# Performance work log

Hardware: AMD Instinct MI355X
Metric: run time of the kernel (lower is better)

## Reference

```python
import jax, jax.numpy as jnp
import numpy as np

B, S, H = 4, 8256, 768
NH, HD = 12, 64
W = 128
SHIFT = W // 2  # 64; first SHIFT tokens form their own block after the shift
NW = (S - SHIFT) // W  # 64 full windows
ROPE_BASE = 10000.0


def _rope_cos_sin(length, hd):
    inv_freq = 1.0 / (ROPE_BASE ** (jnp.arange(0, hd, 2, dtype=jnp.float32) / hd))
    ang = jnp.arange(length, dtype=jnp.float32)[:, None] * inv_freq[None, :]  # [L, hd/2]
    return jnp.cos(ang), jnp.sin(ang)


def _apply_rope(x, cos, sin):
    # x: [..., L, hd]; cos/sin: [L, hd/2] (broadcast over leading dims)
    x1, x2 = x[..., : HD // 2], x[..., HD // 2 :]
    return jnp.concatenate([x1 * cos - x2 * sin, x2 * cos + x1 * sin], axis=-1)


def _sdpa(q, k, v):
    # q,k,v: [..., L, hd]; full softmax attention within the block
    scores = jnp.einsum('...qd,...kd->...qk', q, k) / jnp.sqrt(jnp.asarray(HD, q.dtype))
    probs = jax.nn.softmax(scores, axis=-1)
    return jnp.einsum('...qk,...kd->...qd', probs, v)


def setup_inputs() -> dict:
    key = jax.random.key(0)
    ks = jax.random.split(key, 8)
    std = 0.02
    return {
        'hidden_states': jax.random.normal(ks[0], (B, S, H), dtype=jnp.float32),
        'attention_mask': jnp.zeros((B, 1, 1, S), dtype=jnp.float32),
        'Wq': jax.random.normal(ks[1], (H, H), dtype=jnp.float32) * std,
        'bq': jnp.zeros((H,), dtype=jnp.float32),
        'Wk': jax.random.normal(ks[2], (H, H), dtype=jnp.float32) * std,
        'bk': jnp.zeros((H,), dtype=jnp.float32),
        'Wv': jax.random.normal(ks[3], (H, H), dtype=jnp.float32) * std,
        'bv': jnp.zeros((H,), dtype=jnp.float32),
    }


def _global_block(h, Wq, bq, Wk, bk, Wv, bv):
    # h: [B, L, H]; full attention with global-position RoPE (BertSelfAttention.forward)
    L = h.shape[1]
    cos, sin = _rope_cos_sin(L, HD)

    def heads(x):  # [B, L, H] -> [B, NH, L, HD]
        return x.reshape(B, L, NH, HD).transpose(0, 2, 1, 3)

    q = _apply_rope(heads(h @ Wq.T + bq), cos, sin)
    k = _apply_rope(heads(h @ Wk.T + bk), cos, sin)
    v = heads(h @ Wv.T + bv)
    ctx = _sdpa(q, k, v)  # [B, NH, L, HD]
    return ctx.transpose(0, 2, 1, 3).reshape(B, L, H)


def _local_blocks(h, Wq, bq, Wk, bk, Wv, bv):
    # h: [B, NW*W, H]; per-window attention with window-local RoPE (_mh_local)
    cos, sin = _rope_cos_sin(W, HD)

    def win_heads(x):  # [B, NW*W, H] -> [B, NW, NH, W, HD]
        return x.reshape(B, NW, W, NH, HD).transpose(0, 1, 3, 2, 4)

    q = _apply_rope(win_heads(h @ Wq.T + bq), cos, sin)
    k = _apply_rope(win_heads(h @ Wk.T + bk), cos, sin)
    v = win_heads(h @ Wv.T + bv)
    ctx = _sdpa(q, k, v)  # [B, NW, NH, W, HD]
    return ctx.transpose(0, 1, 3, 2, 4).reshape(B, NW * W, H)


def reference(hidden_states, attention_mask, Wq, bq, Wk, bk, Wv, bv):
    # Shifted local attention: first SHIFT tokens attend among themselves
    # (small global block), the rest is split into NW full windows of size W.
    head = _global_block(hidden_states[:, :SHIFT, :], Wq, bq, Wk, bk, Wv, bv)
    body = _local_blocks(hidden_states[:, SHIFT:, :], Wq, bq, Wk, bk, Wv, bv)
    return jnp.concatenate([head, body], axis=1)  # [B, S, H]
```

## Files before the change

kernel.cpp:

```cpp
#include <hip/hip_runtime.h>
#include <stdint.h>

constexpr int B  = 4, S = 8256, H = 768, NH = 12, HD = 64;
constexpr int M  = B * S;
constexpr int N3 = 3 * H;
constexpr int NWG_GEMM = (M / 128) * (N3 / 128);
constexpr int XQ8 = NWG_GEMM / 8, XR8 = NWG_GEMM % 8;
constexpr long XB_OFF   = 0;
constexpr long XB_BYTES = (long)M * H * 2;
constexpr long W_OFF    = XB_OFF + XB_BYTES;
constexpr long W_BYTES  = (long)N3 * H * 2;
constexpr long ROPE_OFF = W_OFF + W_BYTES;
constexpr long ROPE_BYTES = 128 * 32 * 2 * 4;
constexpr long QKV_OFF  = ROPE_OFF + ROPE_BYTES;
constexpr long QKV_BYTES = (long)M * N3 * 2;
constexpr long WS_NEEDED = QKV_OFF + QKV_BYTES;

typedef __attribute__((ext_vector_type(8))) _Float16 h8;
typedef __attribute__((ext_vector_type(8))) unsigned short us8;
typedef __attribute__((ext_vector_type(4))) float f4;

#define MFMA16(a,b,c) __builtin_amdgcn_mfma_f32_16x16x32_f16((a),(b),(c),0,0,0)
#define GLL16(gp, lp) __builtin_amdgcn_global_load_lds( \
    (__attribute__((address_space(1))) void*)(gp),      \
    (__attribute__((address_space(3))) void*)(lp), 16, 0, 0)

static __device__ __forceinline__ unsigned short f2h(float x) {
  _Float16 h = (_Float16)x;
  return __builtin_bit_cast(unsigned short, h);
}
static __device__ __forceinline__ f4 f4z() { f4 z = {0.f,0.f,0.f,0.f}; return z; }

__global__ __launch_bounds__(256) void prep_kernel(
    const float* __restrict__ X,
    const float* __restrict__ Wq, const float* __restrict__ Wk, const float* __restrict__ Wv,
    unsigned short* __restrict__ Xb, unsigned short* __restrict__ Wcat, float* __restrict__ rope)
{
  int bid = blockIdx.x;
  if (bid < 12384) {
    long base = (long)bid * 2048 + threadIdx.x * 8;
    float4 v0 = *(const float4*)(X + base);
    float4 v1 = *(const float4*)(X + base + 4);
    us8 o;
    o[0]=f2h(v0.x); o[1]=f2h(v0.y); o[2]=f2h(v0.z); o[3]=f2h(v0.w);
    o[4]=f2h(v1.x); o[5]=f2h(v1.y); o[6]=f2h(v1.z); o[7]=f2h(v1.w);
    *(us8*)(Xb + base) = o;
  } else if (bid < 13248) {
    int wb  = bid - 12384;
    int mat = wb / 288;
    int base = (wb % 288) * 2048 + threadIdx.x * 8;
    const float* src = (mat == 0) ? Wq : (mat == 1) ? Wk : Wv;
    float4 v0 = *(const float4*)(src + base);
    float4 v1 = *(const float4*)(src + base + 4);
    us8 o;
    o[0]=f2h(v0.x); o[1]=f2h(v0.y); o[2]=f2h(v0.z); o[3]=f2h(v0.w);
    o[4]=f2h(v1.x); o[5]=f2h(v1.y); o[6]=f2h(v1.z); o[7]=f2h(v1.w);
    *(us8*)(Wcat + (long)mat * 589824 + base) = o;
  } else {
    int t = (bid - 13248) * 256 + threadIdx.x;
    int p = t >> 5, i = t & 31;
    double ang = (double)p * pow(10000.0, -(double)i / 32.0);
    rope[2*t]   = (float)cos(ang);
    rope[2*t+1] = (float)sin(ang);
  }
}

__global__ __launch_bounds__(256) void qkv_gemm(
    const unsigned short* __restrict__ Xb, const unsigned short* __restrict__ Wb,
    const float* __restrict__ bqp, const float* __restrict__ bkp, const float* __restrict__ bvp,
    const float* __restrict__ rope, unsigned short* __restrict__ QKV)
{
  __shared__ __align__(16) unsigned char ldsA[2][16384];
  __shared__ __align__(16) unsigned char ldsB[2][16384];
  const int tid = threadIdx.x, lane = tid & 63, wid = tid >> 6;

  const int bid0 = blockIdx.x;
  const int xcd = bid0 & 7, idx = bid0 >> 3;
  const int wgid = (xcd < XR8 ? xcd * (XQ8 + 1) : XR8 * (XQ8 + 1) + (xcd - XR8) * XQ8) + idx;
  const int mt = wgid / 18;
  const int nt = wgid % 18;
  const long m0 = (long)mt * 128;
  const int  n0 = nt * 128;
  const int wm = wid >> 1, wn = wid & 1;

  f4 acc[4][4];
  #pragma unroll
  for (int i = 0; i < 4; ++i)
    #pragma unroll
    for (int j = 0; j < 4; ++j) acc[i][j] = f4z();

  const char* Xc = (const char*)Xb;
  const char* Wc = (const char*)Wb;

#define STAGE(Abuf, Bbuf, kt) do {                                          \
    const int k0b_ = (kt) * 128;                                            \
    _Pragma("unroll")                                                       \
    for (int i_ = 0; i_ < 4; ++i_) {                                        \
      const int ob_ = ((i_ << 2) + wid) * 1024;      \
      const int o_  = ob_ + lane * 16;                \
      const int row_ = o_ >> 7, cb_ = o_ & 127;                             \
      const int csrc_ = cb_ ^ ((row_ & 7) << 4);      \
      GLL16(Xc + (m0 + row_) * 1536 + k0b_ + csrc_, (Abuf) + ob_);          \
      GLL16(Wc + (long)(n0 + row_) * 1536 + k0b_ + csrc_, (Bbuf) + ob_);    \
    }                                                                       \
  } while (0)

#define COMPUTE(Abuf, Bbuf) do {                                            \
    _Pragma("unroll")                                                       \
    for (int ks_ = 0; ks_ < 2; ++ks_) {                                     \
      h8 a_[4], b_[4];                                                      \
      const int kb_ = ks_ * 64 + ((lane >> 4) << 4);                        \
      _Pragma("unroll")                                                     \
      for (int f_ = 0; f_ < 4; ++f_) {                                      \
        const int ra_ = wm * 64 + f_ * 16 + (lane & 15);                    \
        a_[f_] = *(const h8*)((Abuf) + ra_ * 128 + (kb_ ^ ((ra_ & 7) << 4)));\
        const int rb_ = wn * 64 + f_ * 16 + (lane & 15);                    \
        b_[f_] = *(const h8*)((Bbuf) + rb_ * 128 + (kb_ ^ ((rb_ & 7) << 4)));\
      }                                                                     \
      _Pragma("unroll")                                                     \
      for (int fm_ = 0; fm_ < 4; ++fm_)                                     \
        _Pragma("unroll")                                                   \
        for (int fn_ = 0; fn_ < 4; ++fn_)                                   \
          acc[fm_][fn_] = MFMA16(a_[fm_], b_[fn_], acc[fm_][fn_]);          \
    }                                                                       \
  } while (0)

  unsigned char* A0 = ldsA[0];  unsigned char* A1 = ldsA[1];
  unsigned char* B0 = ldsB[0];  unsigned char* B1 = ldsB[1];

  STAGE(A0, B0, 0);
  #pragma unroll
  for (int kt = 0; kt < 12; kt += 2) {
    STAGE(A1, B1, kt + 1);
    asm volatile("s_waitcnt vmcnt(8)" ::: "memory");
    __builtin_amdgcn_s_barrier();
    asm volatile("" ::: "memory");
    COMPUTE(A0, B0);
    asm volatile("" ::: "memory");
    __builtin_amdgcn_s_barrier();
    if (kt + 2 < 12) {
      STAGE(A0, B0, kt + 2);
      asm volatile("s_waitcnt vmcnt(8)" ::: "memory");
    } else {
      asm volatile("s_waitcnt vmcnt(0)" ::: "memory");
    }
    __builtin_amdgcn_s_barrier();
    asm volatile("" ::: "memory");
    COMPUTE(A1, B1);
    asm volatile("" ::: "memory");
    __builtin_amdgcn_s_barrier();
  }
#undef STAGE
#undef COMPUTE

  const int colb = n0 + wn * 64;
  const int sel = (colb >= 1536) ? 2 : (colb >= 768) ? 1 : 0;
  const float* bias = (sel == 0) ? bqp : (sel == 1) ? bkp : bvp;
  const int hcol = colb % 768;
  float bia[4];
  #pragma unroll
  for (int f = 0; f < 4; ++f) bia[f] = bias[hcol + f * 16 + (lane & 15)];

  #pragma unroll
  for (int fm = 0; fm < 4; ++fm) {
    #pragma unroll
    for (int reg = 0; reg < 4; ++reg) {
      const long m = m0 + wm * 64 + fm * 16 + ((lane >> 4) << 2) + reg;
      const int s = (int)(m % (long)S);
      const int pos = (s < 64) ? s : ((s - 64) & 127);
      unsigned short* orow = QKV + m * N3 + colb;
      if (sel < 2) {
        #pragma unroll
        for (int f = 0; f < 2; ++f) {
          const int d1 = f * 16 + (lane & 15);
          const float c  = rope[(pos * 32 + d1) * 2];
          const float sn = rope[(pos * 32 + d1) * 2 + 1];
          const float x1 = acc[fm][f][reg]     + bia[f];
          const float x2 = acc[fm][f + 2][reg] + bia[f + 2];
          orow[f * 16 + (lane & 15)]       = f2h(x1 * c - x2 * sn);
          orow[(f + 2) * 16 + (lane & 15)] = f2h(x2 * c + x1 * sn);
        }
      } else {
        #pragma unroll
        for (int f = 0; f < 4; ++f)
          orow[f * 16 + (lane & 15)] = f2h(acc[fm][f][reg] + bia[f]);
      }
    }
  }
}

template <int T>
__global__ __launch_bounds__(256) void attn_kernel(
    const unsigned short* __restrict__ QKV, float* __restrict__ out)
{
  constexpr int NF  = T / 16;
  constexpr int NKS = T / 32;
  __shared__ __align__(16) unsigned char sKV[16384];
  __shared__ __align__(16) unsigned char sP[4][8192];

  const int tid = threadIdx.x, lane = tid & 63, w = tid >> 6;
  int bid = blockIdx.x;
  const int h = bid % NH; bid /= NH;
  long row0;
  if (T == 64) row0 = (long)bid * S;
  else { const int ww = bid % 64; const int b = bid / 64; row0 = (long)b * S + 64 + (long)ww * 128; }
  const unsigned short* Qb = QKV + row0 * N3 + h * HD;
  const unsigned short* Kb = Qb + H;
  const unsigned short* Vb = Qb + 2 * H;

  {
    const char* Kc = (const char*)Kb;
    #pragma unroll
    for (int i = 0; i < T / 32; ++i) {
      const int o = i * 4096 + tid * 16;
      const int row = o >> 7, cb = o & 127;
      const int csrc = cb ^ ((row & 7) << 4);
      GLL16(Kc + (long)row * (N3 * 2) + csrc, sKV + o);
    }
  }
  us8 va0, va1, vc0, vc1;
  const bool vload = (2 * lane + 1 < T);
  if (vload) {
    const unsigned short* v0 = Vb + (long)(2 * lane) * N3 + w * 16;
    const unsigned short* v1 = v0 + N3;
    va0 = *(const us8*)(v0);  va1 = *(const us8*)(v0 + 8);
    vc0 = *(const us8*)(v1);  vc1 = *(const us8*)(v1 + 8);
  }
  __syncthreads();

  const bool active = (w * 32 < T);
  f4 acc[2][NF];
  if (active) {
    h8 aq[2][2];
    #pragma unroll
    for (int fm = 0; fm < 2; ++fm)
      #pragma unroll
      for (int ks = 0; ks < 2; ++ks) {
        const long r = w * 32 + fm * 16 + (lane & 15);
        aq[fm][ks] = *(const h8*)(Qb + r * N3 + ks * 32 + ((lane >> 4) << 3));
      }
    #pragma unroll
    for (int i = 0; i < 2; ++i)
      #pragma unroll
      for (int f = 0; f < NF; ++f) acc[i][f] = f4z();

    const int kb0 = (lane >> 4) << 4;
    #pragma unroll
    for (int f = 0; f < NF; ++f) {
      const int rk = f * 16 + (lane & 15);
      const int base = rk * 128, sw = (rk & 7) << 4;
      h8 b0 = *(const h8*)(sKV + base + (kb0 ^ sw));
      h8 b1 = *(const h8*)(sKV + base + ((64 + kb0) ^ sw));
      acc[0][f] = MFMA16(aq[0][0], b0, acc[0][f]);
      acc[0][f] = MFMA16(aq[0][1], b1, acc[0][f]);
      acc[1][f] = MFMA16(aq[1][0], b0, acc[1][f]);
      acc[1][f] = MFMA16(aq[1][1], b1, acc[1][f]);
    }
  }
  __syncthreads();

  if (vload) {
    #pragma unroll
    for (int i = 0; i < 8; ++i) {
      const int d = w * 16 + i, d2 = d + 8;
      *(unsigned*)(sKV + d  * 256 + ((4 * lane) ^ ((d  & 15) << 4))) = (unsigned)va0[i] | ((unsigned)vc0[i] << 16);
      *(unsigned*)(sKV + d2 * 256 + ((4 * lane) ^ ((d2 & 15) << 4))) = (unsigned)va1[i] | ((unsigned)vc1[i] << 16);
    }
  }
  if (active) {
    unsigned char* Pw = sP[w];
    #pragma unroll
    for (int fm = 0; fm < 2; ++fm) {
      #pragma unroll
      for (int reg = 0; reg < 4; ++reg) {
        float mx = -3.0e38f;
        #pragma unroll
        for (int f = 0; f < NF; ++f) mx = fmaxf(mx, acc[fm][f][reg]);
        mx = fmaxf(mx, __shfl_xor(mx, 1));
        mx = fmaxf(mx, __shfl_xor(mx, 2));
        mx = fmaxf(mx, __shfl_xor(mx, 4));
        mx = fmaxf(mx, __shfl_xor(mx, 8));
        float pv[NF], sum = 0.f;
        #pragma unroll
        for (int f = 0; f < NF; ++f) {
          const float p = __expf((acc[fm][f][reg] - mx) * 0.125f);
          pv[f] = p; sum += p;
        }
        sum += __shfl_xor(sum, 1);
        sum += __shfl_xor(sum, 2);
        sum += __shfl_xor(sum, 4);
        sum += __shfl_xor(sum, 8);
        const float inv = 1.0f / sum;
        const int rloc = fm * 16 + ((lane >> 4) << 2) + reg;
        const int swz = (rloc & 7) << 4;
        #pragma unroll
        for (int f = 0; f < NF; ++f) {
          const int cb = (f * 16 + (lane & 15)) * 2;
          *(unsigned short*)(Pw + rloc * 256 + (cb ^ swz)) = f2h(pv[f] * inv);
        }
      }
    }
  }
  __syncthreads();

  if (active) {
    unsigned char* Pw = sP[w];
    f4 acc2[2][4];
    #pragma unroll
    for (int i = 0; i < 2; ++i)
      #pragma unroll
      for (int j = 0; j < 4; ++j) acc2[i][j] = f4z();

    #pragma unroll
    for (int ks = 0; ks < NKS; ++ks) {
      h8 pa[2], vb[4];
      const int kb = ks * 64 + ((lane >> 4) << 4);
      #pragma unroll
      for (int fm = 0; fm < 2; ++fm) {
        const int rp = fm * 16 + (lane & 15);
        pa[fm] = *(const h8*)(Pw + rp * 256 + (kb ^ ((rp & 7) << 4)));
      }
      #pragma unroll
      for (int df = 0; df < 4; ++df) {
        const int d = df * 16 + (lane & 15);
        vb[df] = *(const h8*)(sKV + d * 256 + (kb ^ ((d & 15) << 4)));
      }
      #pragma unroll
      for (int fm = 0; fm < 2; ++fm)
        #pragma unroll
        for (int df = 0; df < 4; ++df)
          acc2[fm][df] = MFMA16(pa[fm], vb[df], acc2[fm][df]);
    }

    float* ob = out + (row0 + w * 32) * H + h * HD;
    #pragma unroll
    for (int fm = 0; fm < 2; ++fm)
      #pragma unroll
      for (int df = 0; df < 4; ++df)
        #pragma unroll
        for (int reg = 0; reg < 4; ++reg) {
          const long r = fm * 16 + ((lane >> 4) << 2) + reg;
          const int c = df * 16 + (lane & 15);
          ob[r * H + c] = acc2[fm][df][reg];
        }
  }
}

extern "C" void kernel_launch(void* const* d_in, const int* in_sizes, int n_in,
                              void* d_out, int out_size, void* d_ws, size_t ws_size,
                              hipStream_t stream) {
  const float* X  = (const float*)d_in[0];
  const float* Wq = (const float*)d_in[2];
  const float* bq = (const float*)d_in[3];
  const float* Wk = (const float*)d_in[4];
  const float* bk = (const float*)d_in[5];
  const float* Wv = (const float*)d_in[6];
  const float* bv = (const float*)d_in[7];
  float* out = (float*)d_out;

  if ((long)ws_size < WS_NEEDED) return;

  char* ws = (char*)d_ws;
  unsigned short* Xb   = (unsigned short*)(ws + XB_OFF);
  unsigned short* Wcat = (unsigned short*)(ws + W_OFF);
  float*          rope = (float*)(ws + ROPE_OFF);
  unsigned short* QKV  = (unsigned short*)(ws + QKV_OFF);

  prep_kernel<<<13264, 256, 0, stream>>>(X, Wq, Wk, Wv, Xb, Wcat, rope);
  qkv_gemm<<<NWG_GEMM, 256, 0, stream>>>(Xb, Wcat, bq, bk, bv, rope, QKV);
  attn_kernel<64><<<B * NH, 256, 0, stream>>>(QKV, out);
  attn_kernel<128><<<B * 64 * NH, 256, 0, stream>>>(QKV, out);
}
```

Measured before the change: 399.9 us.

## Deepen QKV GEMM pipeline to five stages with 64-wide K tiles

The QKV projection GEMM moves from a double-buffered 128-wide K loop to a 5-buffer ring of 64-wide K tiles, keeping four tiles of loads in flight. The A and B tiles for each stage share one buffer, and a new row-pair swizzle keeps LDS reads conflict-free at the narrower width. The goal is to hide global-to-LDS load latency better. In exchange it uses more LDS (80KB vs 64KB), which may lower occupancy, and it does more barriers per unit of work.

```diff
diff --git a/kernel.cpp b/kernel.cpp
--- a/kernel.cpp
+++ b/kernel.cpp
@@ -24,6 +24,7 @@
 #define GLL16(gp, lp) __builtin_amdgcn_global_load_lds( \
     (__attribute__((address_space(1))) void*)(gp),      \
     (__attribute__((address_space(3))) void*)(lp), 16, 0, 0)
+#define WAITV(N) asm volatile("s_waitcnt vmcnt(" #N ")" ::: "memory")
 
 static __device__ __forceinline__ unsigned short f2h(float x) {
   _Float16 h = (_Float16)x;
@@ -70,8 +71,7 @@
     const float* __restrict__ bqp, const float* __restrict__ bkp, const float* __restrict__ bvp,
     const float* __restrict__ rope, unsigned short* __restrict__ QKV)
 {
-  __shared__ __align__(16) unsigned char ldsA[2][16384];
-  __shared__ __align__(16) unsigned char ldsB[2][16384];
+  __shared__ __align__(16) unsigned char lds[5][16384];
   const int tid = threadIdx.x, lane = tid & 63, wid = tid >> 6;
 
   const int bid0 = blockIdx.x;
@@ -92,61 +92,52 @@
   const char* Xc = (const char*)Xb;
   const char* Wc = (const char*)Wb;
 
-#define STAGE(Abuf, Bbuf, kt) do {                                          \
-    const int k0b_ = (kt) * 128;                                            \
+#define STAGE(bi, kt) do {                                                  \
+    const int k0b_ = (kt) * 64;                                             \
+    unsigned char* buf_ = lds[bi];                                          \
     _Pragma("unroll")                                                       \
-    for (int i_ = 0; i_ < 4; ++i_) {                                        \
-      const int ob_ = ((i_ << 2) + wid) * 1024;      \
-      const int o_  = ob_ + lane * 16;                \
-      const int row_ = o_ >> 7, cb_ = o_ & 127;                             \
-      const int csrc_ = cb_ ^ ((row_ & 7) << 4);      \
-      GLL16(Xc + (m0 + row_) * 1536 + k0b_ + csrc_, (Abuf) + ob_);          \
-      GLL16(Wc + (long)(n0 + row_) * 1536 + k0b_ + csrc_, (Bbuf) + ob_);    \
+    for (int i_ = 0; i_ < 2; ++i_) {                                        \
+      const int o_  = i_ * 4096 + tid * 16;           \
+      const int slot_ = o_ >> 7, d_ = o_ & 127;                             \
+      const int row_ = slot_ * 2 + (d_ >> 6), c_ = d_ & 63;                 \
+      const int cs_ = c_ ^ ((slot_ & 3) << 4);        \
+      GLL16(Xc + (m0 + row_) * 1536 + k0b_ + cs_, buf_ + o_);               \
+      GLL16(Wc + (long)(n0 + row_) * 1536 + k0b_ + cs_, buf_ + 8192 + o_);  \
     }                                                                       \
   } while (0)
 
-#define COMPUTE(Abuf, Bbuf) do {                                            \
+#define COMPUTE(bi) do {                                                    \
+    unsigned char* buf_ = lds[bi];                                          \
+    h8 a_[4], b_[4];                                                        \
+    const int kc_ = (lane >> 4) << 4;                                       \
     _Pragma("unroll")                                                       \
-    for (int ks_ = 0; ks_ < 2; ++ks_) {                                     \
-      h8 a_[4], b_[4];                                                      \
-      const int kb_ = ks_ * 64 + ((lane >> 4) << 4);                        \
+    for (int f_ = 0; f_ < 4; ++f_) {                                        \
+      const int ra_ = wm * 64 + f_ * 16 + (lane & 15);                      \
+      a_[f_] = *(const h8*)(buf_ + (ra_ >> 1) * 128 + (ra_ & 1) * 64        \
+                            + (kc_ ^ (((ra_ >> 1) & 3) << 4)));             \
+      const int rb_ = wn * 64 + f_ * 16 + (lane & 15);                      \
+      b_[f_] = *(const h8*)(buf_ + 8192 + (rb_ >> 1) * 128 + (rb_ & 1) * 64 \
+                            + (kc_ ^ (((rb_ >> 1) & 3) << 4)));             \
+    }                                                                       \
+    _Pragma("unroll")                                                       \
+    for (int fm_ = 0; fm_ < 4; ++fm_)                                       \
       _Pragma("unroll")                                                     \
-      for (int f_ = 0; f_ < 4; ++f_) {                                      \
-        const int ra_ = wm * 64 + f_ * 16 + (lane & 15);                    \
-        a_[f_] = *(const h8*)((Abuf) + ra_ * 128 + (kb_ ^ ((ra_ & 7) << 4)));\
-        const int rb_ = wn * 64 + f_ * 16 + (lane & 15);                    \
-        b_[f_] = *(const h8*)((Bbuf) + rb_ * 128 + (kb_ ^ ((rb_ & 7) << 4)));\
-      }                                                                     \
-      _Pragma("unroll")                                                     \
-      for (int fm_ = 0; fm_ < 4; ++fm_)                                     \
-        _Pragma("unroll")                                                   \
-        for (int fn_ = 0; fn_ < 4; ++fn_)                                   \
-          acc[fm_][fn_] = MFMA16(a_[fm_], b_[fn_], acc[fm_][fn_]);          \
-    }                                                                       \
+      for (int fn_ = 0; fn_ < 4; ++fn_)                                     \
+        acc[fm_][fn_] = MFMA16(a_[fm_], b_[fn_], acc[fm_][fn_]);            \
   } while (0)
 
-  unsigned char* A0 = ldsA[0];  unsigned char* A1 = ldsA[1];
-  unsigned char* B0 = ldsB[0];  unsigned char* B1 = ldsB[1];
-
-  STAGE(A0, B0, 0);
+  STAGE(0, 0); STAGE(1, 1); STAGE(2, 2); STAGE(3, 3);
   #pragma unroll
-  for (int kt = 0; kt < 12; kt += 2) {
-    STAGE(A1, B1, kt + 1);
-    asm volatile("s_waitcnt vmcnt(8)" ::: "memory");
+  for (int i = 0; i < 24; ++i) {
+    if (i + 4 < 24) STAGE((i + 4) % 5, i + 4);
+    if (i <= 19)      WAITV(16);
+    else if (i == 20) WAITV(12);
+    else if (i == 21) WAITV(8);
+    else if (i == 22) WAITV(4);
+    else              WAITV(0);
     __builtin_amdgcn_s_barrier();
     asm volatile("" ::: "memory");
-    COMPUTE(A0, B0);
-    asm volatile("" ::: "memory");
-    __builtin_amdgcn_s_barrier();
-    if (kt + 2 < 12) {
-      STAGE(A0, B0, kt + 2);
-      asm volatile("s_waitcnt vmcnt(8)" ::: "memory");
-    } else {
-      asm volatile("s_waitcnt vmcnt(0)" ::: "memory");
-    }
-    __builtin_amdgcn_s_barrier();
-    asm volatile("" ::: "memory");
-    COMPUTE(A1, B1);
+    COMPUTE(i % 5);
     asm volatile("" ::: "memory");
     __builtin_amdgcn_s_barrier();
   }
```

After: 405.7 us. No clear change (+1.4%).
